# Optimization experiments

Hardware: AMD Instinct MI355X
Metric: run time of the kernel (lower is better)

## Reference

```python
import jax, jax.numpy as jnp
import numpy as np

B, T, S, E, H, V = 64, 72, 72, 128, 256, 32000


def setup_inputs() -> dict:
    key = jax.random.key(0)
    ks = jax.random.split(key, 12)
    scale = 1.0 / np.sqrt(H)
    return {
        "target_tensor": jax.random.randint(ks[0], (B, T), 0, V),
        "encoder_outputs": jax.random.normal(ks[1], (B, S, H), dtype=jnp.float32),
        "encoder_seq_lens": jax.random.randint(ks[2], (B,), 1, S + 1),
        "h0": jax.random.normal(ks[3], (B, H), dtype=jnp.float32),
        "c0": jax.random.normal(ks[4], (B, H), dtype=jnp.float32),
        "emb": jax.random.normal(ks[5], (V, E), dtype=jnp.float32) * 0.05,
        "W_ih": jax.random.uniform(ks[6], (4 * H, E), jnp.float32, -scale, scale),
        "W_hh": jax.random.uniform(ks[7], (4 * H, H), jnp.float32, -scale, scale),
        "b_ih": jax.random.uniform(ks[8], (4 * H,), jnp.float32, -scale, scale),
        "b_hh": jax.random.uniform(ks[9], (4 * H,), jnp.float32, -scale, scale),
        "W_lin": jax.random.uniform(ks[10], (V, 2 * H), jnp.float32, -scale, scale),
        "b_lin": jax.random.uniform(ks[11], (V,), jnp.float32, -scale, scale),
    }


def reference(target_tensor, encoder_outputs, encoder_seq_lens, h0, c0,
              emb, W_ih, W_hh, b_ih, b_hh, W_lin, b_lin):
    # attention mask over encoder positions: (B, S) bool
    mask = jnp.arange(S)[None, :] < encoder_seq_lens[:, None]
    inv_sqrt_h = 1.0 / jnp.sqrt(jnp.asarray(H, jnp.float32))
    bias = b_ih + b_hh

    def step(carry, tok):
        h, c = carry                                   # (B,H) each
        x = emb[tok]                                   # (B,E) embedding lookup
        gates = x @ W_ih.T + h @ W_hh.T + bias         # (B,4H), torch gate order i,f,g,o
        i, f, g, o = jnp.split(gates, 4, axis=-1)
        c_new = jax.nn.sigmoid(f) * c + jax.nn.sigmoid(i) * jnp.tanh(g)
        h_new = jax.nn.sigmoid(o) * jnp.tanh(c_new)    # lstm_output for a 1-step LSTM
        scores = jnp.einsum('bh,bsh->bs', h_new, encoder_outputs) * inv_sqrt_h
        scores = jnp.where(mask, scores, -jnp.inf)
        attn = jax.nn.softmax(scores, axis=-1)         # (B,S)
        ctx = jnp.einsum('bs,bsh->bh', attn, encoder_outputs)
        logits = jnp.concatenate([h_new, ctx], axis=-1) @ W_lin.T + b_lin  # (B,V)
        return (h_new, c_new), logits

    (_, _), outs = jax.lax.scan(step, (h0, c0), target_tensor.T)  # outs: (T,B,V)
    return jnp.transpose(outs, (1, 0, 2))              # (B, T, V)
```

## Files before the change

kernel.cpp:

```cpp
#include <hip/hip_runtime.h>

#define BB 64
#define TT 72
#define SS 72
#define EE 128
#define HH 256
#define VV 32000
#define KK 512
#define NB 8
#define NATTN 64
#define NGEMM 184
#define NNT2 63
#define NITEM (36 * NNT2)

using f32x4  = __attribute__((ext_vector_type(4))) float;
using short8 = __attribute__((ext_vector_type(8))) short;
typedef unsigned long long u64;

__device__ __forceinline__ unsigned short f2bf(float f) {
  unsigned u = __float_as_uint(f);
  unsigned r = (u + 0x7fffu + ((u >> 16) & 1u)) >> 16;
  return (unsigned short)r;
}
__device__ __forceinline__ float bf2f(unsigned short b) {
  return __uint_as_float(((unsigned)b) << 16);
}
__device__ __forceinline__ float sigm(float x) { return 1.f / (1.f + __expf(-x)); }
__device__ __forceinline__ float tanh_f(float x) { return 1.f - 2.f / (__expf(2.f * x) + 1.f); }

__device__ __forceinline__ float wsum(float v) {
  v += __shfl_xor(v, 1, 64);  v += __shfl_xor(v, 2, 64);  v += __shfl_xor(v, 4, 64);
  v += __shfl_xor(v, 8, 64);  v += __shfl_xor(v, 16, 64); v += __shfl_xor(v, 32, 64);
  return v;
}
__device__ __forceinline__ float wmax(float v) {
  v = fmaxf(v, __shfl_xor(v, 1, 64));  v = fmaxf(v, __shfl_xor(v, 2, 64));
  v = fmaxf(v, __shfl_xor(v, 4, 64));  v = fmaxf(v, __shfl_xor(v, 8, 64));
  v = fmaxf(v, __shfl_xor(v, 16, 64)); v = fmaxf(v, __shfl_xor(v, 32, 64));
  return v;
}
__device__ __forceinline__ void g2l16(const void* g, void* l) {
  __builtin_amdgcn_global_load_lds((const __attribute__((address_space(1))) void*)g,
                                   (__attribute__((address_space(3))) void*)l, 16, 0, 0);
}
__device__ __forceinline__ uint4 pack8(const float4 v0, const float4 v1) {
  uint4 o;
  o.x = f2bf(v0.x) | ((unsigned)f2bf(v0.y) << 16);
  o.y = f2bf(v0.z) | ((unsigned)f2bf(v0.w) << 16);
  o.z = f2bf(v1.x) | ((unsigned)f2bf(v1.y) << 16);
  o.w = f2bf(v1.z) | ((unsigned)f2bf(v1.w) << 16);
  return o;
}
__device__ __forceinline__ u64 aload(const u64* p) {
  return __hip_atomic_load(p, __ATOMIC_RELAXED, __HIP_MEMORY_SCOPE_AGENT);
}
__device__ __forceinline__ void astore(u64* p, u64 v) {
  __hip_atomic_store(p, v, __ATOMIC_RELAXED, __HIP_MEMORY_SCOPE_AGENT);
}

__global__ void prep_kernel(const int* __restrict__ tok, const float* __restrict__ emb,
                            const float* __restrict__ Wlin,
                            uint4* __restrict__ xembt, unsigned short* __restrict__ wlin16) {
  const int bid = blockIdx.x, tid = threadIdx.x;
  if (bid < 18) {
    for (int e = bid * 256 + tid; e < TT * 16 * 64; e += 18 * 256) {
      const int b = e & 63, kcx = (e >> 6) & 15, t = e >> 10;
      const int tk = tok[b * TT + t];
      const float4* s = (const float4*)(emb + (size_t)tk * EE + kcx * 8);
      xembt[e] = pack8(s[0], s[1]);
    }
  } else {
    const int n4 = (VV * KK) / 4;
    for (int i = (bid - 18) * 256 + tid; i < n4; i += 238 * 256) {
      float4 v = ((const float4*)Wlin)[i];
      ushort4 o;
      o.x = f2bf(v.x); o.y = f2bf(v.y); o.z = f2bf(v.z); o.w = f2bf(v.w);
      ((ushort4*)wlin16)[i] = o;
    }
  }
}

__global__ __launch_bounds__(512) void mega_kernel(
    const float* __restrict__ h0, const float* __restrict__ c0,
    const float* __restrict__ Wih, const float* __restrict__ Whh,
    const float* __restrict__ bih, const float* __restrict__ bhh,
    const float* __restrict__ enc, const int* __restrict__ lens,
    const float* __restrict__ blin, const uint4* __restrict__ xembt,
    const unsigned short* __restrict__ wlin16,
    uint4* __restrict__ hex, unsigned int* __restrict__ sync,
    u64* __restrict__ hcat64, float* __restrict__ out) {
  __shared__ __align__(16) char smem[90112];
  __shared__ int s_role;

  const int tid = threadIdx.x;
  unsigned int* flags1 = sync;
  unsigned int* F2     = sync + 256;
  unsigned int* elect  = sync + 336;

  if (tid == 0) {
    unsigned xcd;
    asm volatile("s_getreg_b32 %0, hwreg(20, 0, 8)" : "=s"(xcd));
    xcd &= 7;
    int role = -1;
    const unsigned my = __hip_atomic_fetch_add(elect + xcd, 1u,
                          __ATOMIC_RELAXED, __HIP_MEMORY_SCOPE_AGENT);
    if (my < NB) {
      if (my == NB - 1) {
        unsigned exp = 0;
        __hip_atomic_compare_exchange_strong(elect + 8, &exp, xcd + 1,
            __ATOMIC_RELAXED, __ATOMIC_RELAXED, __HIP_MEMORY_SCOPE_AGENT);
      }
      unsigned wv;
      while ((wv = __hip_atomic_load(elect + 8, __ATOMIC_RELAXED,
                                     __HIP_MEMORY_SCOPE_AGENT)) == 0)
        __builtin_amdgcn_s_sleep(1);
      if (wv == xcd + 1) role = (int)my;
    }
    if (role < 0) {
      const unsigned idx = __hip_atomic_fetch_add(elect + 9, 1u,
                             __ATOMIC_RELAXED, __HIP_MEMORY_SCOPE_AGENT);
      role = (idx < NATTN) ? (100 + (int)idx) : (1000 + (int)(idx - NATTN));
    }
    s_role = role;
  }
  __syncthreads();
  const int role = s_role;

  if (role < NB) {
    const int bk = role;
    uint4* hx = (uint4*)smem;
    float* biasL = (float*)(smem + 49152);
    const int ln = tid & 63, w = tid >> 6;
    const int n16 = ln & 15, kgrp = ln >> 4;
    const int wj = w >> 2, wb = w & 3;
    u64* hexq = (u64*)hex;

    short8 wf[4][12];
#pragma unroll
    for (int g = 0; g < 4; ++g) {
      const int row = g * HH + bk * 32 + wj * 16 + n16;
#pragma unroll
      for (int kt = 0; kt < 12; ++kt) {
        const float* src = (kt < 8) ? (Whh + (size_t)row * HH + kt * 32 + kgrp * 8)
                                    : (Wih + (size_t)row * EE + (kt - 8) * 32 + kgrp * 8);
        const float4 v0 = ((const float4*)src)[0];
        const float4 v1 = ((const float4*)src)[1];
        short8 wv;
        wv[0]=(short)f2bf(v0.x); wv[1]=(short)f2bf(v0.y); wv[2]=(short)f2bf(v0.z); wv[3]=(short)f2bf(v0.w);
        wv[4]=(short)f2bf(v1.x); wv[5]=(short)f2bf(v1.y); wv[6]=(short)f2bf(v1.z); wv[7]=(short)f2bf(v1.w);
        wf[g][kt] = wv;
      }
    }
    if (tid < 128) {
      const int wj2 = tid >> 6, kg2 = (tid >> 4) & 3, g2 = (tid >> 2) & 3, r2 = tid & 3;
      const int row = g2 * HH + bk * 32 + wj2 * 16 + kg2 * 4 + r2;
      biasL[tid] = bih[row] + bhh[row];
    }
    const int batch = wb * 16 + n16;
    const int j0 = bk * 32 + wj * 16 + kgrp * 4;
    float creg[4];
    {
      const float4 cv = *(const float4*)(c0 + (size_t)batch * HH + j0);
      creg[0] = cv.x; creg[1] = cv.y; creg[2] = cv.z; creg[3] = cv.w;
    }
#pragma unroll
    for (int i = 0; i < 4; ++i) {
      const int e = i * 512 + tid;
      const int kc = e >> 6, b = e & 63;
      const float* src = h0 + (size_t)b * HH + kc * 8;
      hx[kc * 64 + b] = pack8(((const float4*)src)[0], ((const float4*)src)[1]);
    }
    __syncthreads();

    const int kcq  = bk * 4 + wj * 2 + (kgrp >> 1);
    const int half = kgrp & 1;

    for (int t = 0; t < TT; ++t) {
#pragma unroll
      for (int i = 0; i < 2; ++i) {
        const int e = i * 512 + w * 64 + ln;
        g2l16(xembt + (size_t)t * 1024 + e, (char*)hx + (size_t)(2048 + e) * 16);
      }
      if (t > 0) {
        if (tid < NB) {
          while (__hip_atomic_load(flags1 + tid * 32, __ATOMIC_RELAXED,
                                   __HIP_MEMORY_SCOPE_AGENT) < (unsigned)t)
            __builtin_amdgcn_s_sleep(1);
        }
        __syncthreads();
#pragma unroll
        for (int i = 0; i < 4; ++i) {
          const int e = i * 512 + w * 64 + ln;
          g2l16(hex + (size_t)t * 2048 + e, (char*)hx + (size_t)e * 16);
        }
      }
      __syncthreads();

      f32x4 a0 = {0,0,0,0}, a1 = a0, a2 = a0, a3 = a0;
#pragma unroll
      for (int kt = 0; kt < 12; ++kt) {
        const short8 b = *(const short8*)&hx[(kt * 4 + kgrp) * 64 + batch];
        a0 = __builtin_amdgcn_mfma_f32_16x16x32_bf16(wf[0][kt], b, a0, 0, 0, 0);
        a1 = __builtin_amdgcn_mfma_f32_16x16x32_bf16(wf[1][kt], b, a1, 0, 0, 0);
        a2 = __builtin_amdgcn_mfma_f32_16x16x32_bf16(wf[2][kt], b, a2, 0, 0, 0);
        a3 = __builtin_amdgcn_mfma_f32_16x16x32_bf16(wf[3][kt], b, a3, 0, 0, 0);
      }
      const float4 b0 = *(const float4*)&biasL[wj * 64 + kgrp * 16 + 0];
      const float4 b1 = *(const float4*)&biasL[wj * 64 + kgrp * 16 + 4];
      const float4 b2 = *(const float4*)&biasL[wj * 64 + kgrp * 16 + 8];
      const float4 b3 = *(const float4*)&biasL[wj * 64 + kgrp * 16 + 12];
      const float bi[4] = {b0.x, b0.y, b0.z, b0.w};
      const float bf_[4] = {b1.x, b1.y, b1.z, b1.w};
      const float bg[4] = {b2.x, b2.y, b2.z, b2.w};
      const float bo[4] = {b3.x, b3.y, b3.z, b3.w};
      u64 pk = 0;
#pragma unroll
      for (int r = 0; r < 4; ++r) {
        const float iv = a0[r] + bi[r], fv = a1[r] + bf_[r],
                    gv = a2[r] + bg[r], ov = a3[r] + bo[r];
        const float cn = sigm(fv) * creg[r] + sigm(iv) * tanh_f(gv);
        creg[r] = cn;
        const float hv = sigm(ov) * tanh_f(cn);
        pk |= (u64)f2bf(hv) << (16 * r);
      }
      astore(hexq + ((size_t)(t + 1) * 2048 + kcq * 64 + batch) * 2 + half, pk);
      asm volatile("s_waitcnt vmcnt(0)" ::: "memory");
      __syncthreads();
      if (tid == 0)
        __hip_atomic_store(flags1 + bk * 32, (unsigned)(t + 1),
                           __ATOMIC_RELAXED, __HIP_MEMORY_SCOPE_AGENT);
    }
  } else if (role < 1000) {
    const int b = role - 100;
    float* enc_s = (float*)smem;
    float* h_s   = (float*)(smem + 73728);
    float* at_s  = (float*)(smem + 74752);
    float* ctx_s = (float*)(smem + 75776);
    const int wv8 = tid >> 6, ln = tid & 63;
    const int len = lens[b];
    const u64* hexq = (const u64*)hex;
    {
      const float4* src = (const float4*)(enc + (size_t)b * SS * HH);
      float4* dst = (float4*)enc_s;
      for (int i = tid; i < SS * HH / 4; i += 512) dst[i] = src[i];
    }
    __syncthreads();

    for (int t = 0; t < TT; ++t) {
      if (tid < NB) {
        while (__hip_atomic_load(flags1 + tid * 32, __ATOMIC_RELAXED,
                                 __HIP_MEMORY_SCOPE_AGENT) < (unsigned)(t + 1))
          __builtin_amdgcn_s_sleep(1);
      }
      __syncthreads();
      if (tid < 64) {
        const int kc = tid >> 1, hf = tid & 1;
        const u64 v = aload(hexq + ((size_t)(t + 1) * 2048 + kc * 64 + b) * 2 + hf);
        const int j0 = kc * 8 + hf * 4;
        h_s[j0]     = bf2f((unsigned short)v);
        h_s[j0 + 1] = bf2f((unsigned short)(v >> 16));
        h_s[j0 + 2] = bf2f((unsigned short)(v >> 32));
        h_s[j0 + 3] = bf2f((unsigned short)(v >> 48));
        astore(hcat64 + (size_t)(t * 64 + b) * 128 + tid, v);
      }
      __syncthreads();

      const float4 hv = ((const float4*)h_s)[ln];
      for (int s = wv8; s < SS; s += 8) {
        const float4 ev = ((const float4*)(enc_s + s * HH))[ln];
        float p = hv.x * ev.x + hv.y * ev.y + hv.z * ev.z + hv.w * ev.w;
        p = wsum(p);
        if (ln == 0) at_s[s] = p * 0.0625f;
      }
      __syncthreads();
      if (wv8 == 0) {
        const float v0 = (ln < len) ? at_s[ln] : -3.0e38f;
        const bool has1 = (ln < 8) && (64 + ln < len);
        const float v1 = has1 ? at_s[64 + ln] : -3.0e38f;
        const float m = wmax(fmaxf(v0, v1));
        const float e0 = (ln < len) ? __expf(v0 - m) : 0.f;
        const float e1 = has1 ? __expf(v1 - m) : 0.f;
        const float inv = 1.f / wsum(e0 + e1);
        at_s[ln] = e0 * inv;
        if (ln < 8) at_s[64 + ln] = e1 * inv;
      }
      __syncthreads();
      if (tid < HH) {
        float acc = 0.f;
#pragma unroll 8
        for (int s = 0; s < SS; ++s) acc += at_s[s] * enc_s[s * HH + tid];
        ctx_s[tid] = acc;
      }
      __syncthreads();
      if (tid < 64) {
        const u64 pk = (u64)f2bf(ctx_s[tid * 4])
                     | ((u64)f2bf(ctx_s[tid * 4 + 1]) << 16)
                     | ((u64)f2bf(ctx_s[tid * 4 + 2]) << 32)
                     | ((u64)f2bf(ctx_s[tid * 4 + 3]) << 48);
        astore(hcat64 + (size_t)(t * 64 + b) * 128 + 64 + tid, pk);
      }
      asm volatile("s_waitcnt vmcnt(0)" ::: "memory");
      __syncthreads();
      if (tid == 0)
        __hip_atomic_fetch_add(F2 + t, 1u, __ATOMIC_RELAXED, __HIP_MEMORY_SCOPE_AGENT);
    }
  } else {
    const int gid = role - 1000;
    char* AsB = smem;
    char* BsB = smem + 16384;
    const int ln = tid & 63, w = tid >> 6;
    const int n16 = ln & 15, kgrp = ln >> 4;
    const int wm = w >> 2, wn = w & 3;

    for (int it = gid; it < NITEM; it += NGEMM) {
      const int mc = it / NNT2, ntl = it % NNT2;
      if (tid < 2) {
        while (__hip_atomic_load(F2 + 2 * mc + tid, __ATOMIC_RELAXED,
                                 __HIP_MEMORY_SCOPE_AGENT) < NATTN)
          __builtin_amdgcn_s_sleep(8);
      }
      __syncthreads();
      const int m0 = mc * 128, n0 = ntl * 512;
      float bs[8];
#pragma unroll
      for (int f = 0; f < 8; ++f) {
        const int n = n0 + wn * 128 + f * 16 + n16;
        bs[f] = (n < VV) ? blin[n] : 0.f;
      }
      {
        const int row = tid >> 2, sl = tid & 3;
        g2l16((const char*)hcat64 + (size_t)(m0 + row) * 1024 + ((sl ^ (row & 3)) << 4),
              AsB + tid * 16);
      }
#pragma unroll
      for (int i = 0; i < 4; ++i) {
        const int e = i * 512 + tid, row = e >> 2, sl = e & 3;
        g2l16((const char*)wlin16 + (size_t)(n0 + row) * 1024 + ((sl ^ (row & 3)) << 4),
              BsB + e * 16);
      }
      __syncthreads();

      f32x4 acc[4][8] = {};
      for (int kt = 0; kt < 16; ++kt) {
        const int cur = kt & 1;
        if (kt < 15) {
          const int nb = cur ^ 1;
          const int kb = (kt + 1) * 64;
          {
            const int row = tid >> 2, sl = tid & 3;
            g2l16((const char*)hcat64 + (size_t)(m0 + row) * 1024 + kb + ((sl ^ (row & 3)) << 4),
                  AsB + nb * 8192 + tid * 16);
          }
#pragma unroll
          for (int i = 0; i < 4; ++i) {
            const int e = i * 512 + tid, row = e >> 2, sl = e & 3;
            g2l16((const char*)wlin16 + (size_t)(n0 + row) * 1024 + kb + ((sl ^ (row & 3)) << 4),
                  BsB + nb * 32768 + e * 16);
          }
        }
        short8 af[4], bf[8];
#pragma unroll
        for (int f = 0; f < 4; ++f) {
          const int row = wm * 64 + f * 16 + n16;
          af[f] = *(const short8*)(AsB + cur * 8192 + row * 64 + ((kgrp ^ (row & 3)) << 4));
        }
#pragma unroll
        for (int f = 0; f < 8; ++f) {
          const int row = wn * 128 + f * 16 + n16;
          bf[f] = *(const short8*)(BsB + cur * 32768 + row * 64 + ((kgrp ^ (row & 3)) << 4));
        }
#pragma unroll
        for (int fm = 0; fm < 4; ++fm)
#pragma unroll
          for (int fn = 0; fn < 8; ++fn)
            acc[fm][fn] = __builtin_amdgcn_mfma_f32_16x16x32_bf16(af[fm], bf[fn], acc[fm][fn], 0, 0, 0);
        __syncthreads();
      }

      const int trow = mc * 2 + wm;
#pragma unroll
      for (int fm = 0; fm < 4; ++fm) {
        const int b0 = fm * 16 + kgrp * 4;
#pragma unroll
        for (int fn = 0; fn < 8; ++fn) {
          const int n = n0 + wn * 128 + fn * 16 + n16;
          if (n < VV) {
            float* cp = out + ((size_t)b0 * TT + trow) * VV + n;
#pragma unroll
            for (int r = 0; r < 4; ++r) cp[(size_t)r * TT * VV] = acc[fm][fn][r] + bs[fn];
          }
        }
      }
    }
  }
}

extern "C" void kernel_launch(void* const* d_in, const int* in_sizes, int n_in,
                              void* d_out, int out_size, void* d_ws, size_t ws_size,
                              hipStream_t stream) {
  const int*   tok  = (const int*)  d_in[0];
  const float* enc  = (const float*)d_in[1];
  const int*   lens = (const int*)  d_in[2];
  const float* h0   = (const float*)d_in[3];
  const float* c0   = (const float*)d_in[4];
  const float* emb  = (const float*)d_in[5];
  const float* Wih  = (const float*)d_in[6];
  const float* Whh  = (const float*)d_in[7];
  const float* bih  = (const float*)d_in[8];
  const float* bhh  = (const float*)d_in[9];
  const float* Wlin = (const float*)d_in[10];
  const float* blin = (const float*)d_in[11];

  char* ws = (char*)d_ws;
  unsigned short* wlin16 = (unsigned short*)(ws);
  u64*            hcat64 = (u64*)           (ws + 33030144);
  uint4*          xembt  = (uint4*)         (ws + 37748736);
  uint4*          hex    = (uint4*)         (ws + 38928384);
  unsigned int*   sync   = (unsigned int*)  (ws + 41320448);
  float* out = (float*)d_out;

  hipMemsetAsync(sync, 0, 2048, stream);
  prep_kernel<<<256, 256, 0, stream>>>(tok, emb, Wlin, xembt, wlin16);
  mega_kernel<<<256, 512, 0, stream>>>(h0, c0, Wih, Whh, bih, bhh, enc, lens,
                                       blin, xembt, wlin16, hex, sync, hcat64, out);
}
```

Baseline: 546.4 us.

## Overlap recurrent-state fetch with input-projection MFMAs in LSTM step loop

In the persistent LSTM role, every wave now polls the eight step flags itself via a ballot instead of one thread polling and then a block barrier. The gate MFMAs are split so the embedding-input part (kt 8..11) runs while the hidden-state loads are still in flight, using partial vmcnt waits and raw s_barrier. Attention and GEMM roles get longer sleep intervals, and the attention role reads h with a plain load instead of an atomic load. This shortens the serial per-step critical path across CTAs. It relies on vmcnt ordering and on plain-load visibility of cross-CTA data, which could risk stale reads.

```diff
diff --git a/kernel.cpp b/kernel.cpp
--- a/kernel.cpp
+++ b/kernel.cpp
@@ -178,33 +178,50 @@
     for (int t = 0; t < TT; ++t) {
 #pragma unroll
       for (int i = 0; i < 2; ++i) {
-        const int e = i * 512 + w * 64 + ln;
+        const int e = i * 512 + tid;
         g2l16(xembt + (size_t)t * 1024 + e, (char*)hx + (size_t)(2048 + e) * 16);
       }
       if (t > 0) {
-        if (tid < NB) {
-          while (__hip_atomic_load(flags1 + tid * 32, __ATOMIC_RELAXED,
-                                   __HIP_MEMORY_SCOPE_AGENT) < (unsigned)t)
-            __builtin_amdgcn_s_sleep(1);
-        }
-        __syncthreads();
+        for (;;) {
+          unsigned f = 0xffffffffu;
+          if (ln < NB) f = __hip_atomic_load(flags1 + ln * 32, __ATOMIC_RELAXED,
+                                             __HIP_MEMORY_SCOPE_AGENT);
+          if ((__ballot(f >= (unsigned)t) & 0xffull) == 0xffull) break;
+          __builtin_amdgcn_s_sleep(1);
+        }
 #pragma unroll
         for (int i = 0; i < 4; ++i) {
-          const int e = i * 512 + w * 64 + ln;
+          const int e = i * 512 + tid;
           g2l16(hex + (size_t)t * 2048 + e, (char*)hx + (size_t)e * 16);
         }
-      }
-      __syncthreads();
+        asm volatile("s_waitcnt vmcnt(4)" ::: "memory");
+      } else {
+        asm volatile("s_waitcnt vmcnt(0)" ::: "memory");
+      }
+      __builtin_amdgcn_sched_barrier(0);
+      __builtin_amdgcn_s_barrier();
 
       f32x4 a0 = {0,0,0,0}, a1 = a0, a2 = a0, a3 = a0;
 #pragma unroll
-      for (int kt = 0; kt < 12; ++kt) {
+      for (int kt = 8; kt < 12; ++kt) {
         const short8 b = *(const short8*)&hx[(kt * 4 + kgrp) * 64 + batch];
         a0 = __builtin_amdgcn_mfma_f32_16x16x32_bf16(wf[0][kt], b, a0, 0, 0, 0);
         a1 = __builtin_amdgcn_mfma_f32_16x16x32_bf16(wf[1][kt], b, a1, 0, 0, 0);
         a2 = __builtin_amdgcn_mfma_f32_16x16x32_bf16(wf[2][kt], b, a2, 0, 0, 0);
         a3 = __builtin_amdgcn_mfma_f32_16x16x32_bf16(wf[3][kt], b, a3, 0, 0, 0);
       }
+      asm volatile("s_waitcnt vmcnt(0)" ::: "memory");
+      __builtin_amdgcn_sched_barrier(0);
+      __builtin_amdgcn_s_barrier();
+#pragma unroll
+      for (int kt = 0; kt < 8; ++kt) {
+        const short8 b = *(const short8*)&hx[(kt * 4 + kgrp) * 64 + batch];
+        a0 = __builtin_amdgcn_mfma_f32_16x16x32_bf16(wf[0][kt], b, a0, 0, 0, 0);
+        a1 = __builtin_amdgcn_mfma_f32_16x16x32_bf16(wf[1][kt], b, a1, 0, 0, 0);
+        a2 = __builtin_amdgcn_mfma_f32_16x16x32_bf16(wf[2][kt], b, a2, 0, 0, 0);
+        a3 = __builtin_amdgcn_mfma_f32_16x16x32_bf16(wf[3][kt], b, a3, 0, 0, 0);
+      }
+
       const float4 b0 = *(const float4*)&biasL[wj * 64 + kgrp * 16 + 0];
       const float4 b1 = *(const float4*)&biasL[wj * 64 + kgrp * 16 + 4];
       const float4 b2 = *(const float4*)&biasL[wj * 64 + kgrp * 16 + 8];
@@ -225,7 +242,7 @@
       }
       astore(hexq + ((size_t)(t + 1) * 2048 + kcq * 64 + batch) * 2 + half, pk);
       asm volatile("s_waitcnt vmcnt(0)" ::: "memory");
-      __syncthreads();
+      __builtin_amdgcn_s_barrier();
       if (tid == 0)
         __hip_atomic_store(flags1 + bk * 32, (unsigned)(t + 1),
                            __ATOMIC_RELAXED, __HIP_MEMORY_SCOPE_AGENT);
@@ -250,12 +267,12 @@
       if (tid < NB) {
         while (__hip_atomic_load(flags1 + tid * 32, __ATOMIC_RELAXED,
                                  __HIP_MEMORY_SCOPE_AGENT) < (unsigned)(t + 1))
-          __builtin_amdgcn_s_sleep(1);
+          __builtin_amdgcn_s_sleep(2);
       }
       __syncthreads();
       if (tid < 64) {
         const int kc = tid >> 1, hf = tid & 1;
-        const u64 v = aload(hexq + ((size_t)(t + 1) * 2048 + kc * 64 + b) * 2 + hf);
+        const u64 v = hexq[((size_t)(t + 1) * 2048 + kc * 64 + b) * 2 + hf];
         const int j0 = kc * 8 + hf * 4;
         h_s[j0]     = bf2f((unsigned short)v);
         h_s[j0 + 1] = bf2f((unsigned short)(v >> 16));
@@ -317,7 +334,7 @@
       if (tid < 2) {
         while (__hip_atomic_load(F2 + 2 * mc + tid, __ATOMIC_RELAXED,
                                  __HIP_MEMORY_SCOPE_AGENT) < NATTN)
-          __builtin_amdgcn_s_sleep(8);
+          __builtin_amdgcn_s_sleep(16);
       }
       __syncthreads();
       const int m0 = mc * 128, n0 = ntl * 512;
```

Result: faster. 527.7 us (-3.4%).
